# Performance work log

Measured on AMD Instinct MI355X. Metric: run time of the kernel, lower is better.

## Reference

```python
import jax, jax.numpy as jnp
import numpy as np

N_NODES = 100000
N_EDGES = 1600000
IN_CH = 128
OUT_CH = 64
HID = 2 * OUT_CH  # 128


def setup_inputs() -> dict:
    key = jax.random.key(0)
    ks = jax.random.split(key, 8)
    x = jax.random.normal(ks[0], (N_NODES, IN_CH), dtype=jnp.float32)
    edge_index = jax.random.randint(ks[1], (2, N_EDGES), 0, N_NODES, dtype=jnp.int64)

    def glorot(k, shape):
        return jax.random.normal(k, shape, dtype=jnp.float32) / jnp.sqrt(jnp.float32(shape[0]))

    W1 = glorot(ks[2], (IN_CH, HID))
    b1 = jax.random.normal(ks[3], (HID,), dtype=jnp.float32) * 0.01
    W_mu = glorot(ks[4], (HID, OUT_CH))
    b_mu = jax.random.normal(ks[5], (OUT_CH,), dtype=jnp.float32) * 0.01
    W_logstd = glorot(ks[6], (HID, OUT_CH))
    b_logstd = jax.random.normal(ks[7], (OUT_CH,), dtype=jnp.float32) * 0.01
    return {"x": x, "edge_index": edge_index, "W1": W1, "b1": b1,
            "W_mu": W_mu, "b_mu": b_mu, "W_logstd": W_logstd, "b_logstd": b_logstd}


def _gcn_norm(edge_index, n_nodes):
    # PyG GCNConv: add self-loops, symmetric normalization deg^{-1/2} A deg^{-1/2}
    loop = jnp.arange(n_nodes, dtype=edge_index.dtype)
    src = jnp.concatenate([edge_index[0], loop])  # [E+N]
    dst = jnp.concatenate([edge_index[1], loop])  # [E+N]
    deg = jax.ops.segment_sum(jnp.ones_like(dst, dtype=jnp.float32), dst,
                              num_segments=n_nodes)
    dinv = jnp.where(deg > 0, jax.lax.rsqrt(jnp.maximum(deg, 1.0)), 0.0)
    norm = dinv[src] * dinv[dst]  # [E+N]
    return src, dst, norm


def _gcn_conv(x, src, dst, norm, W, b, n_nodes):
    h = x @ W                                   # [N, out] linear first (small out dims)
    msg = h[src] * norm[:, None]                # [E+N, out] gather + scale
    out = jax.ops.segment_sum(msg, dst, num_segments=n_nodes)  # scatter-add
    return out + b


def reference(x, edge_index, W1, b1, W_mu, b_mu, W_logstd, b_logstd):
    n = x.shape[0]
    src, dst, norm = _gcn_norm(edge_index, n)  # same graph for all three layers
    h = jax.nn.relu(_gcn_conv(x, src, dst, norm, W1, b1, n))
    mu = _gcn_conv(h, src, dst, norm, W_mu, b_mu, n)
    logstd = _gcn_conv(h, src, dst, norm, W_logstd, b_logstd, n)
    return mu, logstd
```

## Files before the change

### kernel.cpp

```cpp
#include <hip/hip_runtime.h>
#include <stdint.h>

#define N_NODES 100000
#define N_EDGES 1600000
#define BSHIFT 9
#define NB 196
#define CAP_T 9216
#define CAPP 11264
#define SENT 0x80000000u

typedef __attribute__((ext_vector_type(8))) short short8;
typedef __attribute__((ext_vector_type(4))) float f32x4;
typedef __attribute__((ext_vector_type(2))) float f32x2;
typedef __attribute__((ext_vector_type(4))) unsigned u32x4;
typedef __attribute__((ext_vector_type(2))) unsigned u32x2;
typedef __attribute__((ext_vector_type(4))) int i32x4;

static __device__ __forceinline__ unsigned short f2bf(float f){
  unsigned u = __float_as_uint(f);
  u += 0x7fffu + ((u >> 16) & 1u);
  return (unsigned short)(u >> 16);
}
static __device__ __forceinline__ unsigned pack2bf(float a, float b){
  return (unsigned)f2bf(a) | ((unsigned)f2bf(b) << 16);
}

__global__ __launch_bounds__(256)
void k_init(const float* __restrict__ W1, const float* __restrict__ Wmu,
            const float* __restrict__ Wls, short8* __restrict__ img,
            unsigned* __restrict__ gcur){
  int t = threadIdx.x;
  if (blockIdx.x == 16){
    if (t < NB) gcur[t] = t * CAP_T;
    return;
  }
  int gid = blockIdx.x*256 + t;
  int k = gid >> 11, slot = gid & 2047;
  int lane = slot & 63, ks = (slot >> 6) & 3, tt = slot >> 8;
  int c = tt*16 + (lane & 15);
  int kb = ks*32 + (lane >> 4)*8;
  short8 v;
  #pragma unroll
  for (int j = 0; j < 8; ++j){
    float f;
    if (k == 0) f = W1[(kb + j)*128 + c];
    else        f = (c < 64) ? Wmu[(kb + j)*64 + c] : Wls[(kb + j)*64 + (c - 64)];
    v[j] = (short)f2bf(f);
  }
  img[gid] = v;
}

__global__ __launch_bounds__(256)
void k_binB(const int* __restrict__ ei, unsigned* __restrict__ gcur,
            unsigned* __restrict__ tmp){
  __shared__ unsigned cnt[NB];
  __shared__ unsigned gbase[NB];
  __shared__ unsigned loff[NB];
  __shared__ unsigned sc[256];
  __shared__ unsigned sen[2048];
  __shared__ unsigned spos[2048];
  int t = threadIdx.x;
  for (int j = t; j < NB; j += 256) cnt[j] = 0u;
  __syncthreads();
  unsigned bk[8], rk[8], en[8];
  int e0 = blockIdx.x*2048 + t*8;
  #pragma unroll
  for (int half = 0; half < 2; ++half){
    i32x4 sv, dv;
    bool any = (e0 + half*4) < N_EDGES;
    if (any){
      sv = *(const i32x4*)(ei + e0 + half*4);
      dv = *(const i32x4*)(ei + N_EDGES + e0 + half*4);
    }
    #pragma unroll
    for (int j = 0; j < 4; ++j){
      int q = half*4 + j;
      int e = e0 + q;
      bool ok = e < N_EDGES;
      unsigned d = ok ? (unsigned)dv[j] : 0u;
      unsigned s = ok ? (unsigned)sv[j] : 0u;
      ok = ok && d < N_NODES && s < N_NODES;
      bk[q] = ok ? (d >> BSHIFT) : 0xffffffffu;
      rk[q] = 0u; en[q] = 0u;
      if (ok){ rk[q] = atomicAdd(&cnt[bk[q]], 1u); en[q] = s | ((d & 511u) << 17); }
    }
  }
  __syncthreads();
  sc[t] = (t < NB) ? cnt[t] : 0u;
  __syncthreads();
  for (int off = 1; off < 256; off <<= 1){
    unsigned a = (t >= off) ? sc[t - off] : 0u;
    __syncthreads();
    sc[t] += a;
    __syncthreads();
  }
  if (t < NB){
    loff[t]  = sc[t] - cnt[t];
    gbase[t] = cnt[t] ? atomicAdd(&gcur[t], cnt[t]) : 0u;
  }
  __syncthreads();
  unsigned total = sc[NB - 1];
  #pragma unroll
  for (int j = 0; j < 8; ++j)
    if (bk[j] != 0xffffffffu){
      unsigned lp = loff[bk[j]] + rk[j];
      unsigned gp = gbase[bk[j]] + rk[j];
      sen[lp]  = en[j];
      spos[lp] = (gp < (bk[j] + 1u)*CAP_T) ? gp : 0xffffffffu;
    }
  __syncthreads();
  for (unsigned idx = t; idx < total; idx += 256){
    unsigned p = spos[idx];
    if (p != 0xffffffffu) tmp[p] = sen[idx];
  }
}

__global__ __launch_bounds__(256)
void k_binC(const unsigned* __restrict__ gcur, const unsigned* __restrict__ tmp,
            unsigned* __restrict__ csr, unsigned* __restrict__ begdeg,
            float* __restrict__ dinv){
  __shared__ unsigned cnt[512];
  __shared__ unsigned cur[512];
  __shared__ unsigned sc[512];
  int b = blockIdx.x, t = threadIdx.x;
  unsigned base_t = (unsigned)b * CAP_T;
  unsigned basep  = (unsigned)b * CAPP;
  unsigned sz = min(gcur[b] - base_t, (unsigned)CAP_T);
  cnt[t] = 0u; cnt[t + 256] = 0u;
  __syncthreads();
  for (unsigned idx = t; idx < sz; idx += 256)
    atomicAdd(&cnt[(tmp[base_t + idx] >> 17) & 511u], 1u);
  __syncthreads();
  unsigned c0 = cnt[t], c1 = cnt[t + 256];
  unsigned p0 = (c0 + 7u) & ~7u, p1 = (c1 + 7u) & ~7u;
  sc[t] = p0; sc[t + 256] = p1;
  __syncthreads();
  for (int off = 1; off < 512; off <<= 1){
    unsigned a0 = (t >= off)       ? sc[t - off]       : 0u;
    unsigned a1 = (t + 256 >= off) ? sc[t + 256 - off] : 0u;
    __syncthreads();
    sc[t] += a0; sc[t + 256] += a1;
    __syncthreads();
  }
  unsigned e0 = sc[t] - p0, e1 = sc[t + 256] - p1;
  cur[t] = e0; cur[t + 256] = e1;
  {
    int n0 = b*512 + t, n1 = n0 + 256;
    if (n0 < N_NODES){
      begdeg[n0] = (((basep + e0) >> 3) << 11) | min(c0, 2047u);
      dinv[n0] = rsqrtf((float)(c0 + 1u));
      for (unsigned k = c0; k < p0; ++k) csr[basep + e0 + k] = SENT;
    }
    if (n1 < N_NODES){
      begdeg[n1] = (((basep + e1) >> 3) << 11) | min(c1, 2047u);
      dinv[n1] = rsqrtf((float)(c1 + 1u));
      for (unsigned k = c1; k < p1; ++k) csr[basep + e1 + k] = SENT;
    }
  }
  __syncthreads();
  for (unsigned idx = t; idx < sz; idx += 256){
    unsigned en = tmp[base_t + idx];
    unsigned p = atomicAdd(&cur[(en >> 17) & 511u], 1u);
    if (p < (unsigned)CAPP) csr[basep + p] = en;
  }
}

__global__ __launch_bounds__(256)
void k_pack(const unsigned* __restrict__ csr, const float* __restrict__ dinv,
            u32x2* __restrict__ csr2){
  unsigned e = blockIdx.x*256 + threadIdx.x;
  if (e >= (unsigned)NB*CAPP) return;
  unsigned en = csr[e];
  u32x2 v;
  if (en & SENT){ v[0] = 0u; v[1] = 0u; }
  else {
    unsigned src = min(en & 0x1FFFFu, (unsigned)(N_NODES - 1));
    v[0] = src; v[1] = __float_as_uint(dinv[src]);
  }
  csr2[e] = v;
}

template<bool AF32>
__global__ __launch_bounds__(256)
void k_gemm(const void* __restrict__ A_, const short8* __restrict__ img,
            unsigned short* __restrict__ out, int M)
{
  __shared__ short8 wf[2048];
  int tid = threadIdx.x;
  #pragma unroll
  for (int s = 0; s < 8; ++s) wf[tid + 256*s] = img[tid + 256*s];
  __syncthreads();

  int wave = tid >> 6, lane = tid & 63;
  int rb = blockIdx.x*128 + wave*32;
  int r0 = rb + (lane & 15);
  int r1 = r0 + 16;
  int ra0 = min(r0, M-1), ra1 = min(r1, M-1);
  int koff = (lane >> 4)*8;

  short8 a0[4], a1[4];
  if (AF32){
    const float* A = (const float*)A_;
    #pragma unroll
    for (int ks = 0; ks < 4; ++ks){
      const float* p0 = A + (size_t)ra0*128 + ks*32 + koff;
      const float* p1 = A + (size_t)ra1*128 + ks*32 + koff;
      f32x4 xa = *(const f32x4*)p0, xb = *(const f32x4*)(p0 + 4);
      f32x4 ya = *(const f32x4*)p1, yb = *(const f32x4*)(p1 + 4);
      short8 t0, t1;
      #pragma unroll
      for (int j = 0; j < 4; ++j){
        t0[j] = (short)f2bf(xa[j]); t0[j+4] = (short)f2bf(xb[j]);
        t1[j] = (short)f2bf(ya[j]); t1[j+4] = (short)f2bf(yb[j]);
      }
      a0[ks] = t0; a1[ks] = t1;
    }
  } else {
    const unsigned short* A = (const unsigned short*)A_;
    #pragma unroll
    for (int ks = 0; ks < 4; ++ks){
      a0[ks] = *(const short8*)(A + (size_t)ra0*128 + ks*32 + koff);
      a1[ks] = *(const short8*)(A + (size_t)ra1*128 + ks*32 + koff);
    }
  }

  f32x4 acc[2][8];
  #pragma unroll
  for (int t = 0; t < 8; ++t){ acc[0][t] = (f32x4)0.f; acc[1][t] = (f32x4)0.f; }

  #pragma unroll
  for (int t = 0; t < 8; ++t){
    #pragma unroll
    for (int ks = 0; ks < 4; ++ks){
      short8 b = wf[(t*4 + ks)*64 + lane];
      acc[0][t] = __builtin_amdgcn_mfma_f32_16x16x32_bf16(a0[ks], b, acc[0][t], 0, 0, 0);
      acc[1][t] = __builtin_amdgcn_mfma_f32_16x16x32_bf16(a1[ks], b, acc[1][t], 0, 0, 0);
    }
  }

  #pragma unroll
  for (int sub = 0; sub < 2; ++sub){
    int rbase = rb + sub*16 + (lane >> 4)*4;
    int c = lane & 15;
    #pragma unroll
    for (int t = 0; t < 8; ++t){
      #pragma unroll
      for (int j = 0; j < 4; ++j){
        int r = rbase + j;
        if (r < M) out[(size_t)r*128 + t*16 + c] = f2bf(acc[sub][t][j]);
      }
    }
  }
}

template<int MODE>
__global__ __launch_bounds__(256)
void k_agg(const unsigned short* __restrict__ hin, const unsigned* __restrict__ begdeg,
           const u32x2* __restrict__ csr2, const float* __restrict__ dinv,
           const float* __restrict__ bias, const float* __restrict__ bias2,
           unsigned* __restrict__ out_bf, float* __restrict__ out_f)
{
  int i = blockIdx.x*4 + (threadIdx.x >> 6);
  int lane = threadIdx.x & 63;
  int slot = lane >> 4, c8 = lane & 15;
  float di = dinv[i];

  f32x2 acc2[4];
  {
    u32x4 sv = *(const u32x4*)(hin + (size_t)i*128 + c8*8);
    float ws = (slot == 0) ? di*di : 0.f;
    #pragma unroll
    for (int j = 0; j < 4; ++j){
      acc2[j].x = ws * __uint_as_float(sv[j] << 16);
      acc2[j].y = ws * __uint_as_float(sv[j] & 0xffff0000u);
    }
  }

  unsigned pk = begdeg[i];
  unsigned beg = (pk >> 11) << 3;
  int nit = ((int)(pk & 2047u) + 7) >> 3;

  const u32x4* ep = (const u32x4*)(csr2 + beg + 2*slot);
  u32x4 eA = ep[0];
  u32x4 eB = ep[4];
  u32x4 rA0 = *(const u32x4*)(hin + (size_t)eA[0]*128 + c8*8);
  u32x4 rA1 = *(const u32x4*)(hin + (size_t)eA[2]*128 + c8*8);

  for (int it = 0; it < nit; ++it){
    u32x4 eC = ep[4*it + 8];
    u32x4 rB0 = *(const u32x4*)(hin + (size_t)eB[0]*128 + c8*8);
    u32x4 rB1 = *(const u32x4*)(hin + (size_t)eB[2]*128 + c8*8);

    f32x2 w0v; w0v.x = di * __uint_as_float(eA[1]); w0v.y = w0v.x;
    f32x2 w1v; w1v.x = di * __uint_as_float(eA[3]); w1v.y = w1v.x;
    #pragma unroll
    for (int j = 0; j < 4; ++j){
      f32x2 v0; v0.x = __uint_as_float(rA0[j] << 16); v0.y = __uint_as_float(rA0[j] & 0xffff0000u);
      f32x2 v1; v1.x = __uint_as_float(rA1[j] << 16); v1.y = __uint_as_float(rA1[j] & 0xffff0000u);
      acc2[j] = __builtin_elementwise_fma(w0v, v0, acc2[j]);
      acc2[j] = __builtin_elementwise_fma(w1v, v1, acc2[j]);
    }

    eA = eB; eB = eC; rA0 = rB0; rA1 = rB1;
  }

  #pragma unroll
  for (int j = 0; j < 4; ++j){
    acc2[j].x += __shfl_xor(acc2[j].x, 16);
    acc2[j].x += __shfl_xor(acc2[j].x, 32);
    acc2[j].y += __shfl_xor(acc2[j].y, 16);
    acc2[j].y += __shfl_xor(acc2[j].y, 32);
  }

  if (slot != 0) return;
  int c0 = c8*8;
  if (MODE == 0){
    u32x4 o;
    #pragma unroll
    for (int j = 0; j < 4; ++j){
      float lo = fmaxf(acc2[j].x + bias[c0 + 2*j],     0.f);
      float hi = fmaxf(acc2[j].y + bias[c0 + 2*j + 1], 0.f);
      o[j] = pack2bf(lo, hi);
    }
    *(u32x4*)(out_bf + (size_t)i*64 + c8*4) = o;
  } else {
    const float* bsrc = (c8 < 8) ? (bias + c0) : (bias2 + (c0 - 64));
    float* base = (c8 < 8) ? (out_f + (size_t)i*64 + c0)
                           : (out_f + (size_t)N_NODES*64 + (size_t)i*64 + (c0 - 64));
    f32x4 o0, o1;
    o0[0] = acc2[0].x + bsrc[0]; o0[1] = acc2[0].y + bsrc[1];
    o0[2] = acc2[1].x + bsrc[2]; o0[3] = acc2[1].y + bsrc[3];
    o1[0] = acc2[2].x + bsrc[4]; o1[1] = acc2[2].y + bsrc[5];
    o1[2] = acc2[3].x + bsrc[6]; o1[3] = acc2[3].y + bsrc[7];
    __builtin_nontemporal_store(o0, (f32x4*)base);
    __builtin_nontemporal_store(o1, (f32x4*)(base + 4));
  }
}


extern "C" void kernel_launch(void* const* d_in, const int* in_sizes, int n_in,
                              void* d_out, int out_size, void* d_ws, size_t ws_size,
                              hipStream_t stream)
{
  const float* x   = (const float*)d_in[0];
  const int*   ei  = (const int*)d_in[1];
  const float* W1  = (const float*)d_in[2];
  const float* b1  = (const float*)d_in[3];
  const float* Wmu = (const float*)d_in[4];
  const float* bmu = (const float*)d_in[5];
  const float* Wls = (const float*)d_in[6];
  const float* bls = (const float*)d_in[7];
  float* out = (float*)d_out;

  char* ws = (char*)d_ws;
  unsigned* begdeg = (unsigned*)ws;  ws += 400128;
  float*    dinv   = (float*)ws;     ws += 400128;
  unsigned* gcur   = (unsigned*)ws;  ws += 1024;
  short8*   imgW   = (short8*)ws;    ws += 65536;
  unsigned* csr    = (unsigned*)ws;  ws += (size_t)NB*CAPP*4;
  u32x2*    csr2   = (u32x2*)ws;     ws += (size_t)NB*CAPP*8 + 512;
  char*     shared = ws;             ws += 25600000;
  if (ws_size < (size_t)(ws - (char*)d_ws)) return;
  unsigned*       tmp  = (unsigned*)shared;
  unsigned short* bufA = (unsigned short*)shared;
  unsigned* bufB = (unsigned*)d_out;

  k_init<<<17, 256, 0, stream>>>(W1, Wmu, Wls, imgW, gcur);
  k_binB<<<(N_EDGES + 2047)/2048, 256, 0, stream>>>(ei, gcur, tmp);
  k_binC<<<NB, 256, 0, stream>>>(gcur, tmp, csr, begdeg, dinv);
  k_pack<<<(NB*CAPP + 255)/256, 256, 0, stream>>>(csr, dinv, csr2);

  k_gemm<true ><<<(N_NODES + 127)/128, 256, 0, stream>>>(x, imgW, bufA, N_NODES);
  k_agg<0><<<N_NODES/4, 256, 0, stream>>>(bufA, begdeg, csr2, dinv, b1, nullptr,
                                          bufB, nullptr);
  k_gemm<false><<<(N_NODES + 127)/128, 256, 0, stream>>>((unsigned short*)bufB, imgW + 2048,
                                                         bufA, N_NODES);
  k_agg<1><<<N_NODES/4, 256, 0, stream>>>(bufA, begdeg, csr2, dinv, bmu, bls,
                                          nullptr, out);
}
```

Measured before the change: 220.1 us.

## Quantize GEMM outputs to int8 with per-row scale folded with dinv

Result: faster. 197.4 us (-10.3%).

```diff
diff --git a/kernel.cpp b/kernel.cpp
--- a/kernel.cpp
+++ b/kernel.cpp
@@ -24,14 +24,29 @@
 static __device__ __forceinline__ unsigned pack2bf(float a, float b){
   return (unsigned)f2bf(a) | ((unsigned)f2bf(b) << 16);
 }
+static __device__ __forceinline__ void upk8(u32x2 r, f32x2 w, f32x2* acc){
+  #pragma unroll
+  for (int b = 0; b < 2; ++b){
+    unsigned u = r[b];
+    f32x2 p0, p1;
+    p0.x = (float)(int)(signed char)(u);
+    p0.y = (float)(int)(signed char)(u >> 8);
+    p1.x = (float)(int)(signed char)(u >> 16);
+    p1.y = (float)(int)(signed char)(u >> 24);
+    acc[2*b]     = __builtin_elementwise_fma(w, p0, acc[2*b]);
+    acc[2*b + 1] = __builtin_elementwise_fma(w, p1, acc[2*b + 1]);
+  }
+}
 
 __global__ __launch_bounds__(256)
 void k_init(const float* __restrict__ W1, const float* __restrict__ Wmu,
             const float* __restrict__ Wls, short8* __restrict__ img,
-            unsigned* __restrict__ gcur){
+            unsigned* __restrict__ gcur, float* __restrict__ dsc1,
+            float* __restrict__ dsc2){
   int t = threadIdx.x;
   if (blockIdx.x == 16){
     if (t < NB) gcur[t] = t * CAP_T;
+    if (t == 0){ dsc1[N_NODES] = 0.f; dsc2[N_NODES] = 0.f; }
     return;
   }
   int gid = blockIdx.x*256 + t;
@@ -166,24 +181,18 @@
 }
 
 __global__ __launch_bounds__(256)
-void k_pack(const unsigned* __restrict__ csr, const float* __restrict__ dinv,
-            u32x2* __restrict__ csr2){
+void k_pack(const unsigned* __restrict__ csr, unsigned* __restrict__ csr2){
   unsigned e = blockIdx.x*256 + threadIdx.x;
   if (e >= (unsigned)NB*CAPP) return;
   unsigned en = csr[e];
-  u32x2 v;
-  if (en & SENT){ v[0] = 0u; v[1] = 0u; }
-  else {
-    unsigned src = min(en & 0x1FFFFu, (unsigned)(N_NODES - 1));
-    v[0] = src; v[1] = __float_as_uint(dinv[src]);
-  }
-  csr2[e] = v;
+  csr2[e] = (en & SENT) ? (unsigned)N_NODES : (en & 0x1FFFFu);
 }
 
 template<bool AF32>
 __global__ __launch_bounds__(256)
 void k_gemm(const void* __restrict__ A_, const short8* __restrict__ img,
-            unsigned short* __restrict__ out, int M)
+            signed char* __restrict__ out8, float* __restrict__ dscale,
+            const float* __restrict__ dinv, int M)
 {
   __shared__ short8 wf[2048];
   int tid = threadIdx.x;
@@ -240,14 +249,23 @@
 
   #pragma unroll
   for (int sub = 0; sub < 2; ++sub){
-    int rbase = rb + sub*16 + (lane >> 4)*4;
-    int c = lane & 15;
-    #pragma unroll
-    for (int t = 0; t < 8; ++t){
+    #pragma unroll
+    for (int j = 0; j < 4; ++j){
+      float m = 0.f;
       #pragma unroll
-      for (int j = 0; j < 4; ++j){
-        int r = rbase + j;
-        if (r < M) out[(size_t)r*128 + t*16 + c] = f2bf(acc[sub][t][j]);
+      for (int t = 0; t < 8; ++t) m = fmaxf(m, fabsf(acc[sub][t][j]));
+      #pragma unroll
+      for (int off = 1; off < 16; off <<= 1) m = fmaxf(m, __shfl_xor(m, off));
+      int r = rb + sub*16 + (lane >> 4)*4 + j;
+      if (r < M){
+        float inv = 127.f / fmaxf(m, 1e-20f);
+        #pragma unroll
+        for (int t = 0; t < 8; ++t){
+          int q = __float2int_rn(acc[sub][t][j] * inv);
+          q = max(-127, min(127, q));
+          out8[(size_t)r*128 + t*16 + (lane & 15)] = (signed char)q;
+        }
+        if ((lane & 15) == 0) dscale[r] = dinv[r] * m * (1.f/127.f);
       }
     }
   }
@@ -255,8 +273,9 @@
 
 template<int MODE>
 __global__ __launch_bounds__(256)
-void k_agg(const unsigned short* __restrict__ hin, const unsigned* __restrict__ begdeg,
-           const u32x2* __restrict__ csr2, const float* __restrict__ dinv,
+void k_agg(const signed char* __restrict__ hin, const unsigned* __restrict__ begdeg,
+           const unsigned* __restrict__ csr2, const float* __restrict__ dinv,
+           const float* __restrict__ dscale,
            const float* __restrict__ bias, const float* __restrict__ bias2,
            unsigned* __restrict__ out_bf, float* __restrict__ out_f)
 {
@@ -266,42 +285,38 @@
   float di = dinv[i];
 
   f32x2 acc2[4];
+  #pragma unroll
+  for (int j = 0; j < 4; ++j){ acc2[j].x = 0.f; acc2[j].y = 0.f; }
   {
-    u32x4 sv = *(const u32x4*)(hin + (size_t)i*128 + c8*8);
-    float ws = (slot == 0) ? di*di : 0.f;
-    #pragma unroll
-    for (int j = 0; j < 4; ++j){
-      acc2[j].x = ws * __uint_as_float(sv[j] << 16);
-      acc2[j].y = ws * __uint_as_float(sv[j] & 0xffff0000u);
-    }
+    u32x2 sv = *(const u32x2*)(hin + (size_t)i*128 + c8*8);
+    float ws = (slot == 0) ? di * dscale[i] : 0.f;
+    f32x2 wsv; wsv.x = ws; wsv.y = ws;
+    upk8(sv, wsv, acc2);
   }
 
   unsigned pk = begdeg[i];
   unsigned beg = (pk >> 11) << 3;
   int nit = ((int)(pk & 2047u) + 7) >> 3;
 
-  const u32x4* ep = (const u32x4*)(csr2 + beg + 2*slot);
-  u32x4 eA = ep[0];
-  u32x4 eB = ep[4];
-  u32x4 rA0 = *(const u32x4*)(hin + (size_t)eA[0]*128 + c8*8);
-  u32x4 rA1 = *(const u32x4*)(hin + (size_t)eA[2]*128 + c8*8);
+  const u32x2* ep = (const u32x2*)(csr2 + beg + 2*slot);
+  u32x2 eA = ep[0];
+  u32x2 eB = ep[4];
+  float dsA0 = dscale[eA[0]], dsA1 = dscale[eA[1]];
+  u32x2 rA0 = *(const u32x2*)(hin + (size_t)eA[0]*128 + c8*8);
+  u32x2 rA1 = *(const u32x2*)(hin + (size_t)eA[1]*128 + c8*8);
 
   for (int it = 0; it < nit; ++it){
-    u32x4 eC = ep[4*it + 8];
-    u32x4 rB0 = *(const u32x4*)(hin + (size_t)eB[0]*128 + c8*8);
-    u32x4 rB1 = *(const u32x4*)(hin + (size_t)eB[2]*128 + c8*8);
-
-    f32x2 w0v; w0v.x = di * __uint_as_float(eA[1]); w0v.y = w0v.x;
-    f32x2 w1v; w1v.x = di * __uint_as_float(eA[3]); w1v.y = w1v.x;
-    #pragma unroll
-    for (int j = 0; j < 4; ++j){
-      f32x2 v0; v0.x = __uint_as_float(rA0[j] << 16); v0.y = __uint_as_float(rA0[j] & 0xffff0000u);
-      f32x2 v1; v1.x = __uint_as_float(rA1[j] << 16); v1.y = __uint_as_float(rA1[j] & 0xffff0000u);
-      acc2[j] = __builtin_elementwise_fma(w0v, v0, acc2[j]);
-      acc2[j] = __builtin_elementwise_fma(w1v, v1, acc2[j]);
-    }
-
-    eA = eB; eB = eC; rA0 = rB0; rA1 = rB1;
+    u32x2 eC = ep[4*it + 8];
+    float dsB0 = dscale[eB[0]], dsB1 = dscale[eB[1]];
+    u32x2 rB0 = *(const u32x2*)(hin + (size_t)eB[0]*128 + c8*8);
+    u32x2 rB1 = *(const u32x2*)(hin + (size_t)eB[1]*128 + c8*8);
+
+    f32x2 w0; w0.x = di * dsA0; w0.y = w0.x;
+    f32x2 w1; w1.x = di * dsA1; w1.y = w1.x;
+    upk8(rA0, w0, acc2);
+    upk8(rA1, w1, acc2);
+
+    eA = eB; eB = eC; dsA0 = dsB0; dsA1 = dsB1; rA0 = rB0; rA1 = rB1;
   }
 
   #pragma unroll
@@ -353,28 +368,30 @@
   float* out = (float*)d_out;
 
   char* ws = (char*)d_ws;
-  unsigned* begdeg = (unsigned*)ws;  ws += 400128;
-  float*    dinv   = (float*)ws;     ws += 400128;
-  unsigned* gcur   = (unsigned*)ws;  ws += 1024;
-  short8*   imgW   = (short8*)ws;    ws += 65536;
-  unsigned* csr    = (unsigned*)ws;  ws += (size_t)NB*CAPP*4;
-  u32x2*    csr2   = (u32x2*)ws;     ws += (size_t)NB*CAPP*8 + 512;
-  char*     shared = ws;             ws += 25600000;
+  unsigned*    begdeg = (unsigned*)ws;  ws += 400128;
+  float*       dinv   = (float*)ws;     ws += 400128;
+  float*       dsc1   = (float*)ws;     ws += 400128;
+  float*       dsc2   = (float*)ws;     ws += 400128;
+  unsigned*    gcur   = (unsigned*)ws;  ws += 1024;
+  short8*      imgW   = (short8*)ws;    ws += 65536;
+  unsigned*    csr    = (unsigned*)ws;  ws += (size_t)NB*CAPP*4;
+  unsigned*    csr2   = (unsigned*)ws;  ws += (size_t)NB*CAPP*4 + 512;
+  char*        shared = ws;             ws += 12800256;
   if (ws_size < (size_t)(ws - (char*)d_ws)) return;
-  unsigned*       tmp  = (unsigned*)shared;
-  unsigned short* bufA = (unsigned short*)shared;
+  unsigned*    tmp  = (unsigned*)shared;
+  signed char* bufA = (signed char*)shared;
   unsigned* bufB = (unsigned*)d_out;
 
-  k_init<<<17, 256, 0, stream>>>(W1, Wmu, Wls, imgW, gcur);
+  k_init<<<17, 256, 0, stream>>>(W1, Wmu, Wls, imgW, gcur, dsc1, dsc2);
   k_binB<<<(N_EDGES + 2047)/2048, 256, 0, stream>>>(ei, gcur, tmp);
   k_binC<<<NB, 256, 0, stream>>>(gcur, tmp, csr, begdeg, dinv);
-  k_pack<<<(NB*CAPP + 255)/256, 256, 0, stream>>>(csr, dinv, csr2);
-
-  k_gemm<true ><<<(N_NODES + 127)/128, 256, 0, stream>>>(x, imgW, bufA, N_NODES);
-  k_agg<0><<<N_NODES/4, 256, 0, stream>>>(bufA, begdeg, csr2, dinv, b1, nullptr,
+  k_pack<<<(NB*CAPP + 255)/256, 256, 0, stream>>>(csr, csr2);
+
+  k_gemm<true ><<<(N_NODES + 127)/128, 256, 0, stream>>>(x, imgW, bufA, dsc1, dinv, N_NODES);
+  k_agg<0><<<N_NODES/4, 256, 0, stream>>>(bufA, begdeg, csr2, dinv, dsc1, b1, nullptr,
                                           bufB, nullptr);
   k_gemm<false><<<(N_NODES + 127)/128, 256, 0, stream>>>((unsigned short*)bufB, imgW + 2048,
-                                                         bufA, N_NODES);
-  k_agg<1><<<N_NODES/4, 256, 0, stream>>>(bufA, begdeg, csr2, dinv, bmu, bls,
+                                                         bufA, dsc2, dinv, N_NODES);
+  k_agg<1><<<N_NODES/4, 256, 0, stream>>>(bufA, begdeg, csr2, dinv, dsc2, bmu, bls,
                                           nullptr, out);
 }
```
